# Kernel tuning notes

Hardware: AMD Instinct MI355X
Metric: run time of the kernel (lower is better)

## Reference

```python
import jax, jax.numpy as jnp
import numpy as np

B, T, D = 4, 4096, 512

def setup_inputs() -> dict:
    key = jax.random.key(0)
    k1, k2, k3 = jax.random.split(key, 3)
    z_hat = jax.random.normal(k1, (B, T, D), dtype=jnp.float32)
    P = jax.random.uniform(k2, (B, T), dtype=jnp.float32)
    lengths = jax.random.randint(k3, (B,), 0, T).astype(jnp.int32)
    return {"z_hat": z_hat, "P": P, "lengths": lengths}

def reference(z_hat, P, lengths):
    # z_hat: [B, T, D], P: [B, T], lengths: [B]
    Bs, Tc, _ = z_hat.shape
    P_clamped = jnp.clip(P, 0.0, 1.0 - 1e-6)
    q = 1.0 - P_clamped
    # inclusive cumulative sum of log q (same as padded-cumsum[:,1:] in torch)
    log_cumprod_q = jnp.cumsum(jnp.log(q), axis=1)                 # [B, T]
    log_P = jnp.log(jnp.clip(P_clamped, 1e-6, None))               # [B, T]
    # log_M[b, t, k] = log P[b, k] + logcum[b, t] - logcum[b, k], causal (k <= t)
    log_M = (log_P[:, None, :]
             + log_cumprod_q[:, :, None]
             - log_cumprod_q[:, None, :])                          # [B, T, T]
    t_idx = jnp.arange(Tc)
    causal = t_idx[:, None] >= t_idx[None, :]                      # k <= t kept
    M = jnp.where(causal[None, :, :], jnp.exp(log_M), 0.0)         # [B, T, T]
    z_bar = jnp.einsum('btk,bkd->btd', M, z_hat)                   # [B, T, D]
    padding_mask = t_idx[None, :] < lengths[:, None]               # [B, T]
    return z_bar * padding_mask[:, :, None].astype(z_bar.dtype)
```

## Files before the change

### kernel.cpp

```cpp
#include <hip/hip_runtime.h>


#define CHUNK 16
#define NCMAX 512

__global__ __launch_bounds__(128) void k_local(
    const float* __restrict__ z, const float* __restrict__ P,
    const int* __restrict__ lengths,
    float* __restrict__ S, float* __restrict__ A,
    int B, int T, int D, int NC) {
  int blk = blockIdx.x;
  int b = blk / NC, c = blk % NC;
  int t0 = c * CHUNK;
  int tid = threadIdx.x;
  int D4 = D >> 2;
  float4* S4 = (float4*)(S + ((size_t)b * NC + c) * D);
  int L = lengths[b];
  if (t0 >= L) {
    float4 zero = make_float4(0.f, 0.f, 0.f, 0.f);
    for (int d4 = tid; d4 < D4; d4 += blockDim.x) S4[d4] = zero;
    if (tid == 0) A[b * NC + c] = 1.0f;
    return;
  }
  __shared__ float p_s[CHUNK], q_s[CHUNK];
  if (tid < CHUNK) {
    int tg = t0 + tid;
    float p = (tg < T) ? P[(size_t)b * T + tg] : 0.0f;
    p = fminf(fmaxf(p, 0.0f), 1.0f - 1e-6f);
    q_s[tid] = 1.0f - p;
    p_s[tid] = fmaxf(p, 1e-6f);
  }
  __syncthreads();
  int nt = min(CHUNK, T - t0);
  const float4* z4 = (const float4*)(z + ((size_t)b * T + t0) * D);
  for (int d4 = tid; d4 < D4; d4 += blockDim.x) {
    float4 s = make_float4(0.f, 0.f, 0.f, 0.f);
#pragma unroll
    for (int t = 0; t < CHUNK; ++t) {
      if (t < nt) {
        float4 zv = z4[(size_t)t * D4 + d4];
        float q = q_s[t], pe = p_s[t];
        s.x = fmaf(q, s.x, pe * zv.x);
        s.y = fmaf(q, s.y, pe * zv.y);
        s.z = fmaf(q, s.z, pe * zv.z);
        s.w = fmaf(q, s.w, pe * zv.w);
      }
    }
    S4[d4] = s;
  }
  if (tid == 0) {
    float r = 1.0f;
    for (int t = 0; t < nt; ++t) r *= q_s[t];
    A[b * NC + c] = r;
  }
}

__global__ void k_carry(
    const float* __restrict__ S, const float* __restrict__ A,
    float* __restrict__ Carry, int D4, int NC) {
  int b = blockIdx.x / D4;
  int d4 = blockIdx.x % D4;
  int c = threadIdx.x;
  __shared__ float sh_a[NCMAX];
  __shared__ float4 sh_v[NCMAX];
  float a = A[b * NC + c];
  const float4* S4 = (const float4*)S;
  float4 sv = S4[((size_t)b * NC + c) * D4 + d4];
  sh_a[c] = a;
  sh_v[c] = sv;
  __syncthreads();
  for (int off = 1; off < NC; off <<= 1) {
    float ap = 1.0f;
    float4 vp = make_float4(0.f, 0.f, 0.f, 0.f);
    bool has = (c >= off);
    if (has) { ap = sh_a[c - off]; vp = sh_v[c - off]; }
    __syncthreads();
    if (has) {
      sv.x = fmaf(a, vp.x, sv.x);
      sv.y = fmaf(a, vp.y, sv.y);
      sv.z = fmaf(a, vp.z, sv.z);
      sv.w = fmaf(a, vp.w, sv.w);
      a *= ap;
      sh_a[c] = a;
      sh_v[c] = sv;
    }
    __syncthreads();
  }
  float4 car = make_float4(0.f, 0.f, 0.f, 0.f);
  if (c > 0) car = sh_v[c - 1];
  float4* C4 = (float4*)Carry;
  C4[((size_t)b * NC + c) * D4 + d4] = car;
}

__global__ __launch_bounds__(128) void k_apply(
    const float* __restrict__ z, const float* __restrict__ P,
    const float* __restrict__ Carry, const int* __restrict__ lengths,
    float* __restrict__ out,
    int B, int T, int D, int NC) {
  int blk = blockIdx.x;
  int b = blk / NC, c = blk % NC;
  int t0 = c * CHUNK;
  int tid = threadIdx.x;
  int D4 = D >> 2;
  int nt = min(CHUNK, T - t0);
  float4* o4 = (float4*)(out + ((size_t)b * T + t0) * D);
  int L = lengths[b];
  if (t0 >= L) {
    float4 zero = make_float4(0.f, 0.f, 0.f, 0.f);
    for (int t = 0; t < nt; ++t)
      for (int d4 = tid; d4 < D4; d4 += blockDim.x)
        o4[(size_t)t * D4 + d4] = zero;
    return;
  }
  __shared__ float p_s[CHUNK], q_s[CHUNK];
  if (tid < CHUNK) {
    int tg = t0 + tid;
    float p = (tg < T) ? P[(size_t)b * T + tg] : 0.0f;
    p = fminf(fmaxf(p, 0.0f), 1.0f - 1e-6f);
    q_s[tid] = 1.0f - p;
    p_s[tid] = fmaxf(p, 1e-6f);
  }
  __syncthreads();
  const float4* z4 = (const float4*)(z + ((size_t)b * T + t0) * D);
  const float4* C4 = (const float4*)(Carry + ((size_t)b * NC + c) * D);
  for (int d4 = tid; d4 < D4; d4 += blockDim.x) {
    float4 s = C4[d4];
#pragma unroll
    for (int t = 0; t < CHUNK; ++t) {
      if (t < nt) {
        float4 zv = z4[(size_t)t * D4 + d4];
        float q = q_s[t], pe = p_s[t];
        s.x = fmaf(q, s.x, pe * zv.x);
        s.y = fmaf(q, s.y, pe * zv.y);
        s.z = fmaf(q, s.z, pe * zv.z);
        s.w = fmaf(q, s.w, pe * zv.w);
        float4 o = ((t0 + t) < L) ? s : make_float4(0.f, 0.f, 0.f, 0.f);
        o4[(size_t)t * D4 + d4] = o;
      }
    }
  }
}

extern "C" void kernel_launch(void* const* d_in, const int* in_sizes, int n_in,
                              void* d_out, int out_size, void* d_ws, size_t ws_size,
                              hipStream_t stream) {
  const float* z = (const float*)d_in[0];
  const float* P = (const float*)d_in[1];
  const int* lengths = (const int*)d_in[2];
  float* out = (float*)d_out;

  int B = in_sizes[2];
  int T = in_sizes[1] / B;
  int D = in_sizes[0] / in_sizes[1];
  int NC = (T + CHUNK - 1) / CHUNK;
  int D4 = D >> 2;

  float* S = (float*)d_ws;
  float* A = S + (size_t)B * NC * D;
  float* Carry = A + (((size_t)B * NC + 3) & ~(size_t)3);

  k_local<<<dim3(B * NC), dim3(128), 0, stream>>>(z, P, lengths, S, A, B, T, D, NC);
  k_carry<<<dim3(B * D4), dim3(NC), 0, stream>>>(S, A, Carry, D4, NC);
  k_apply<<<dim3(B * NC), dim3(128), 0, stream>>>(z, P, Carry, lengths, out, B, T, D, NC);
}
```

Measured before the change: 105.1 us.

## Fuse chunked scan into one cooperative kernel with grid syncs and register-held z

Replaces the three-kernel chunked scan (local reduce, carry scan, apply) with a single cooperative kernel. Grid-wide syncs separate the phases. Each thread keeps its 16 z rows in registers, so the apply phase does not read z from memory a second time. The carry scan now pairs chunks before a Hillis-Steele scan over 128 threads and stores carries in a transposed layout. The cost is two grid barriers, higher register pressure, and a requirement that all 1024 blocks be co-resident; if the cooperative launch fails, the code falls back to the three-kernel path.

```diff
diff --git a/kernel.cpp b/kernel.cpp
--- a/kernel.cpp
+++ b/kernel.cpp
@@ -1,8 +1,146 @@
 #include <hip/hip_runtime.h>
+#include <hip/hip_cooperative_groups.h>
+
+namespace cg = cooperative_groups;
 
 
 #define CHUNK 16
 #define NCMAX 512
+
+__global__ __launch_bounds__(128, 2) void k_fused(
+    const float* __restrict__ z, const float* __restrict__ P,
+    const int* __restrict__ lengths,
+    float* __restrict__ S, float* __restrict__ A, float* __restrict__ Carry,
+    float* __restrict__ out, int B, int T, int D4, int NC) {
+  cg::grid_group grid = cg::this_grid();
+  const int blk = blockIdx.x;
+  const int b = blk / NC, c = blk % NC;
+  const int t0 = c * CHUNK;
+  const int tid = threadIdx.x;
+  const int L = lengths[b];
+  const int nt = min(CHUNK, T - t0);
+  const bool masked = (t0 >= L);
+
+  __shared__ float p_s[CHUNK], q_s[CHUNK];
+  __shared__ float sh_a[128];
+  __shared__ float4 sh_s[128];
+
+  const float4 zero = make_float4(0.f, 0.f, 0.f, 0.f);
+  float4 zreg[CHUNK];
+  const float4* z4 = (const float4*)z;
+  float4* o4 = (float4*)out;
+  const size_t zbase = ((size_t)b * T + t0) * D4;
+
+  if (tid < CHUNK) {
+    int tg = t0 + tid;
+    float p = (tg < T && !masked) ? P[(size_t)b * T + tg] : 0.0f;
+    p = fminf(fmaxf(p, 0.0f), 1.0f - 1e-6f);
+    q_s[tid] = 1.0f - p;
+    p_s[tid] = fmaxf(p, 1e-6f);
+  }
+  __syncthreads();
+
+  float4 s = zero;
+  if (tid < D4) {
+    if (!masked) {
+#pragma unroll
+      for (int t = 0; t < CHUNK; ++t)
+        if (t < nt) zreg[t] = z4[zbase + (size_t)t * D4 + tid];
+#pragma unroll
+      for (int t = 0; t < CHUNK; ++t)
+        if (t < nt) {
+          float q = q_s[t], pe = p_s[t];
+          s.x = fmaf(q, s.x, pe * zreg[t].x);
+          s.y = fmaf(q, s.y, pe * zreg[t].y);
+          s.z = fmaf(q, s.z, pe * zreg[t].z);
+          s.w = fmaf(q, s.w, pe * zreg[t].w);
+        }
+    } else {
+      for (int t = 0; t < nt; ++t) o4[zbase + (size_t)t * D4 + tid] = zero;
+    }
+    ((float4*)S)[((size_t)b * NC + c) * D4 + tid] = s;
+  }
+  if (tid == 0) {
+    float a = 1.0f;
+    if (!masked)
+      for (int t = 0; t < nt; ++t) a *= q_s[t];
+    A[b * NC + c] = a;
+  }
+
+  grid.sync();
+
+  {
+    const int ntask = B * D4;
+    if (blk < ntask) {
+      const int tb = blk / D4, td4 = blk % D4;
+      const int half = NC >> 1;
+      float a0 = 1.f, pa = 1.f;
+      float4 s0 = zero, ps = zero;
+      if (tid < half) {
+        int c0 = 2 * tid, c1 = c0 + 1;
+        a0 = A[tb * NC + c0];
+        float a1 = A[tb * NC + c1];
+        s0 = ((const float4*)S)[((size_t)tb * NC + c0) * D4 + td4];
+        float4 s1 = ((const float4*)S)[((size_t)tb * NC + c1) * D4 + td4];
+        pa = a1 * a0;
+        ps.x = fmaf(a1, s0.x, s1.x);
+        ps.y = fmaf(a1, s0.y, s1.y);
+        ps.z = fmaf(a1, s0.z, s1.z);
+        ps.w = fmaf(a1, s0.w, s1.w);
+        sh_a[tid] = pa;
+        sh_s[tid] = ps;
+      }
+      __syncthreads();
+      for (int off = 1; off < half; off <<= 1) {
+        float Ap = 1.f;
+        float4 Sp = zero;
+        bool has = (tid >= off) && (tid < half);
+        if (has) { Ap = sh_a[tid - off]; Sp = sh_s[tid - off]; }
+        __syncthreads();
+        if (has) {
+          ps.x = fmaf(pa, Sp.x, ps.x);
+          ps.y = fmaf(pa, Sp.y, ps.y);
+          ps.z = fmaf(pa, Sp.z, ps.z);
+          ps.w = fmaf(pa, Sp.w, ps.w);
+          pa *= Ap;
+          sh_a[tid] = pa;
+          sh_s[tid] = ps;
+        }
+        __syncthreads();
+      }
+      if (tid < half) {
+        float4 Pp = (tid > 0) ? sh_s[tid - 1] : zero;
+        float4* C4 = (float4*)Carry;
+        size_t base = ((size_t)tb * D4 + td4) * NC;
+        C4[base + 2 * tid] = Pp;
+        float4 c1v;
+        c1v.x = fmaf(a0, Pp.x, s0.x);
+        c1v.y = fmaf(a0, Pp.y, s0.y);
+        c1v.z = fmaf(a0, Pp.z, s0.z);
+        c1v.w = fmaf(a0, Pp.w, s0.w);
+        C4[base + 2 * tid + 1] = c1v;
+      }
+    }
+  }
+
+  grid.sync();
+
+  if (!masked && tid < D4) {
+    float4 sc = ((const float4*)Carry)[((size_t)b * D4 + tid) * NC + c];
+#pragma unroll
+    for (int t = 0; t < CHUNK; ++t)
+      if (t < nt) {
+        float q = q_s[t], pe = p_s[t];
+        sc.x = fmaf(q, sc.x, pe * zreg[t].x);
+        sc.y = fmaf(q, sc.y, pe * zreg[t].y);
+        sc.z = fmaf(q, sc.z, pe * zreg[t].z);
+        sc.w = fmaf(q, sc.w, pe * zreg[t].w);
+        float4 o = ((t0 + t) < L) ? sc : zero;
+        o4[zbase + (size_t)t * D4 + tid] = o;
+      }
+  }
+}
+
 
 __global__ __launch_bounds__(128) void k_local(
     const float* __restrict__ z, const float* __restrict__ P,
@@ -159,6 +297,17 @@
   float* A = S + (size_t)B * NC * D;
   float* Carry = A + (((size_t)B * NC + 3) & ~(size_t)3);
 
+  if ((D & 3) == 0 && D4 >= 64 && D4 <= 128 && NC >= 2 && NC <= 256 &&
+      (NC & 1) == 0 && (size_t)B * NC <= 1024) {
+    void* args[] = {(void*)&z, (void*)&P, (void*)&lengths, (void*)&S, (void*)&A,
+                    (void*)&Carry, (void*)&out, (void*)&B, (void*)&T, (void*)&D4,
+                    (void*)&NC};
+    hipError_t e = hipLaunchCooperativeKernel((const void*)k_fused, dim3(B * NC),
+                                              dim3(128), args, 0, stream);
+    if (e == hipSuccess) return;
+    (void)hipGetLastError();
+  }
+
   k_local<<<dim3(B * NC), dim3(128), 0, stream>>>(z, P, lengths, S, A, B, T, D, NC);
   k_carry<<<dim3(B * D4), dim3(NC), 0, stream>>>(S, A, Carry, D4, NC);
   k_apply<<<dim3(B * NC), dim3(128), 0, stream>>>(z, P, Carry, lengths, out, B, T, D, NC);
```

New measurement: 311.0 us. +195.8%, slower.

## Replace carry-scan kernel with per-chunk weighted sum of previous chunk states

Applied to the files above, without the earlier changes.

Drops the separate scan kernel and its Carry buffer. Each apply block builds suffix products of chunk decay factors with an in-block scan, then forms its incoming carry directly as a weighted sum of all earlier chunk states. The local kernel now keeps the chunk's z rows in registers and writes zeros straight to the output for chunks past the valid length. This removes one launch and the barrier-heavy carry scan, but it adds quadratic, L2-bound reads of the chunk-state buffer for late chunks.

```diff
diff --git a/kernel.cpp b/kernel.cpp
--- a/kernel.cpp
+++ b/kernel.cpp
@@ -5,6 +5,156 @@
 #define NCMAX 512
 
 __global__ __launch_bounds__(128) void k_local(
+    const float* __restrict__ z, const float* __restrict__ P,
+    const int* __restrict__ lengths,
+    float* __restrict__ S, float* __restrict__ A,
+    float* __restrict__ out, int B, int T, int D4, int NC) {
+  const int blk = blockIdx.x;
+  const int b = blk / NC, c = blk % NC;
+  const int t0 = c * CHUNK;
+  const int tid = threadIdx.x;
+  const int L = lengths[b];
+  const int nt = min(CHUNK, T - t0);
+  const float4 zero = make_float4(0.f, 0.f, 0.f, 0.f);
+  const size_t rowbase = ((size_t)b * T + t0) * D4;
+
+  if (t0 >= L) {
+    float4* o4 = (float4*)out;
+    if (tid < D4)
+      for (int t = 0; t < nt; ++t) o4[rowbase + (size_t)t * D4 + tid] = zero;
+    return;
+  }
+
+  __shared__ float p_s[CHUNK], q_s[CHUNK];
+  if (tid < CHUNK) {
+    int tg = t0 + tid;
+    float p = (tg < T) ? P[(size_t)b * T + tg] : 0.0f;
+    p = fminf(fmaxf(p, 0.0f), 1.0f - 1e-6f);
+    q_s[tid] = 1.0f - p;
+    p_s[tid] = fmaxf(p, 1e-6f);
+  }
+  __syncthreads();
+
+  if (tid < D4) {
+    const float4* z4 = (const float4*)z;
+    float4 zr[CHUNK];
+#pragma unroll
+    for (int t = 0; t < CHUNK; ++t)
+      if (t < nt) zr[t] = z4[rowbase + (size_t)t * D4 + tid];
+    float4 s = zero;
+#pragma unroll
+    for (int t = 0; t < CHUNK; ++t)
+      if (t < nt) {
+        float q = q_s[t], pe = p_s[t];
+        s.x = fmaf(q, s.x, pe * zr[t].x);
+        s.y = fmaf(q, s.y, pe * zr[t].y);
+        s.z = fmaf(q, s.z, pe * zr[t].z);
+        s.w = fmaf(q, s.w, pe * zr[t].w);
+      }
+    ((float4*)S)[((size_t)b * NC + c) * D4 + tid] = s;
+  }
+  if (tid == 0) {
+    float r = 1.0f;
+    for (int t = 0; t < nt; ++t) r *= q_s[t];
+    A[b * NC + c] = r;
+  }
+}
+
+__global__ __launch_bounds__(128) void k_apply(
+    const float* __restrict__ z, const float* __restrict__ P,
+    const float* __restrict__ S, const float* __restrict__ A,
+    const int* __restrict__ lengths, float* __restrict__ out,
+    int B, int T, int D4, int NC) {
+  const int blk = blockIdx.x;
+  const int b = blk / NC, c = blk % NC;
+  const int t0 = c * CHUNK;
+  const int tid = threadIdx.x;
+  const int L = lengths[b];
+  if (t0 >= L) return;
+  const int nt = min(CHUNK, T - t0);
+  const float4 zero = make_float4(0.f, 0.f, 0.f, 0.f);
+
+  __shared__ float p_s[CHUNK], q_s[CHUNK];
+  __shared__ float a_s[256];
+  __shared__ float w_s[256];
+
+  if (tid < CHUNK) {
+    int tg = t0 + tid;
+    float p = (tg < T) ? P[(size_t)b * T + tg] : 0.0f;
+    p = fminf(fmaxf(p, 0.0f), 1.0f - 1e-6f);
+    q_s[tid] = 1.0f - p;
+    p_s[tid] = fmaxf(p, 1e-6f);
+  }
+  for (int i = tid; i < NC; i += 128) a_s[i] = A[b * NC + i];
+  __syncthreads();
+
+  {
+    int i0 = tid, i1 = tid + 128;
+    w_s[i0] = (i0 < c - 1) ? a_s[i0 + 1] : 1.0f;
+    w_s[i1] = (i1 < c - 1) ? a_s[i1 + 1] : 1.0f;
+    __syncthreads();
+#pragma unroll
+    for (int off = 1; off < 256; off <<= 1) {
+      float v0 = (i0 + off < 256) ? w_s[i0 + off] : 1.0f;
+      float v1 = (i1 + off < 256) ? w_s[i1 + off] : 1.0f;
+      __syncthreads();
+      w_s[i0] *= v0;
+      w_s[i1] *= v1;
+      __syncthreads();
+    }
+  }
+
+  if (tid < D4) {
+    const float4* S4 = (const float4*)S + (size_t)b * NC * D4 + tid;
+    float4 a0 = zero, a1 = zero, a2 = zero, a3 = zero;
+    int cp = 0;
+    for (; cp + 4 <= c; cp += 4) {
+      float w0 = w_s[cp], w1 = w_s[cp + 1], w2 = w_s[cp + 2], w3 = w_s[cp + 3];
+      float4 r0 = S4[(size_t)cp * D4];
+      float4 r1 = S4[(size_t)(cp + 1) * D4];
+      float4 r2 = S4[(size_t)(cp + 2) * D4];
+      float4 r3 = S4[(size_t)(cp + 3) * D4];
+      a0.x = fmaf(w0, r0.x, a0.x); a0.y = fmaf(w0, r0.y, a0.y);
+      a0.z = fmaf(w0, r0.z, a0.z); a0.w = fmaf(w0, r0.w, a0.w);
+      a1.x = fmaf(w1, r1.x, a1.x); a1.y = fmaf(w1, r1.y, a1.y);
+      a1.z = fmaf(w1, r1.z, a1.z); a1.w = fmaf(w1, r1.w, a1.w);
+      a2.x = fmaf(w2, r2.x, a2.x); a2.y = fmaf(w2, r2.y, a2.y);
+      a2.z = fmaf(w2, r2.z, a2.z); a2.w = fmaf(w2, r2.w, a2.w);
+      a3.x = fmaf(w3, r3.x, a3.x); a3.y = fmaf(w3, r3.y, a3.y);
+      a3.z = fmaf(w3, r3.z, a3.z); a3.w = fmaf(w3, r3.w, a3.w);
+    }
+    for (; cp < c; ++cp) {
+      float w = w_s[cp];
+      float4 r = S4[(size_t)cp * D4];
+      a0.x = fmaf(w, r.x, a0.x); a0.y = fmaf(w, r.y, a0.y);
+      a0.z = fmaf(w, r.z, a0.z); a0.w = fmaf(w, r.w, a0.w);
+    }
+    float4 s;
+    s.x = (a0.x + a1.x) + (a2.x + a3.x);
+    s.y = (a0.y + a1.y) + (a2.y + a3.y);
+    s.z = (a0.z + a1.z) + (a2.z + a3.z);
+    s.w = (a0.w + a1.w) + (a2.w + a3.w);
+
+    const size_t rowbase = ((size_t)b * T + t0) * D4;
+    const float4* z4 = (const float4*)z;
+    float4* o4 = (float4*)out;
+#pragma unroll
+    for (int t = 0; t < CHUNK; ++t)
+      if (t < nt) {
+        float4 zv = z4[rowbase + (size_t)t * D4 + tid];
+        float q = q_s[t], pe = p_s[t];
+        s.x = fmaf(q, s.x, pe * zv.x);
+        s.y = fmaf(q, s.y, pe * zv.y);
+        s.z = fmaf(q, s.z, pe * zv.z);
+        s.w = fmaf(q, s.w, pe * zv.w);
+        float4 o = ((t0 + t) < L) ? s : zero;
+        o4[rowbase + (size_t)t * D4 + tid] = o;
+      }
+  }
+}
+
+
+__global__ __launch_bounds__(128) void f_local(
     const float* __restrict__ z, const float* __restrict__ P,
     const int* __restrict__ lengths,
     float* __restrict__ S, float* __restrict__ A,
@@ -55,7 +205,7 @@
   }
 }
 
-__global__ void k_carry(
+__global__ void f_carry(
     const float* __restrict__ S, const float* __restrict__ A,
     float* __restrict__ Carry, int D4, int NC) {
   int b = blockIdx.x / D4;
@@ -92,7 +242,7 @@
   C4[((size_t)b * NC + c) * D4 + d4] = car;
 }
 
-__global__ __launch_bounds__(128) void k_apply(
+__global__ __launch_bounds__(128) void f_apply(
     const float* __restrict__ z, const float* __restrict__ P,
     const float* __restrict__ Carry, const int* __restrict__ lengths,
     float* __restrict__ out,
@@ -159,7 +309,14 @@
   float* A = S + (size_t)B * NC * D;
   float* Carry = A + (((size_t)B * NC + 3) & ~(size_t)3);
 
-  k_local<<<dim3(B * NC), dim3(128), 0, stream>>>(z, P, lengths, S, A, B, T, D, NC);
-  k_carry<<<dim3(B * D4), dim3(NC), 0, stream>>>(S, A, Carry, D4, NC);
-  k_apply<<<dim3(B * NC), dim3(128), 0, stream>>>(z, P, Carry, lengths, out, B, T, D, NC);
-}
+  if ((D & 3) == 0 && D4 >= 1 && D4 <= 128 && NC >= 1 && NC <= 256) {
+    dim3 grid(B * NC), block(128);
+    k_local<<<grid, block, 0, stream>>>(z, P, lengths, S, A, out, B, T, D4, NC);
+    k_apply<<<grid, block, 0, stream>>>(z, P, S, A, lengths, out, B, T, D4, NC);
+    return;
+  }
+
+  f_local<<<dim3(B * NC), dim3(128), 0, stream>>>(z, P, lengths, S, A, B, T, D, NC);
+  f_carry<<<dim3(B * D4), dim3(NC), 0, stream>>>(S, A, Carry, D4, NC);
+  f_apply<<<dim3(B * NC), dim3(128), 0, stream>>>(z, P, Carry, lengths, out, B, T, D, NC);
+}
```

Measured after the change: 105.2 us. Within noise of the previous version (+0.1%).
